# Kernel optimization log

Measured on AMD Instinct MI355X. Metric: run time of the kernel, lower is better.

## Reference

```python
import jax, jax.numpy as jnp
import numpy as np

B, T, N, D_IN, H, K, E, L = 32, 12, 2000, 2, 64, 2, 10, 2


def setup_inputs() -> dict:
    key = jax.random.key(0)
    ks = jax.random.split(key, 2 + 4 * L)
    s = 0.05
    inp = {
        "x": jax.random.normal(ks[0], (B, T, N, D_IN), jnp.float32),
        "node_embeddings": jax.random.normal(ks[1], (N, E), jnp.float32),
    }
    dims_in = [D_IN, H]
    for l in range(L):
        din = dims_in[l] + H  # cell input is concat([x_t, state])
        inp[f"gate_w{l}"] = jax.random.normal(ks[2 + 4 * l], (E, K, din, 2 * H), jnp.float32) * s
        inp[f"gate_b{l}"] = jax.random.normal(ks[3 + 4 * l], (E, 2 * H), jnp.float32) * s
        inp[f"upd_w{l}"] = jax.random.normal(ks[4 + 4 * l], (E, K, din, H), jnp.float32) * s
        inp[f"upd_b{l}"] = jax.random.normal(ks[5 + 4 * l], (E, H), jnp.float32) * s
    return inp


def _supports(node_embeddings):
    # adaptive adjacency from node embeddings + Chebyshev-style link polynomials
    A = jax.nn.softmax(jax.nn.relu(node_embeddings @ node_embeddings.T), axis=1)  # [N,N]
    sup = [jnp.eye(N, dtype=A.dtype), A]
    for _ in range(K - 2):
        sup.append(2.0 * (A @ sup[-1]) - sup[-2])
    return jnp.stack(sup)  # [K,N,N]


def _gconv(x, supports, emb, w_pool, b_pool):
    # x: [B,N,C] -> [B,N,O]; per-node weights generated from embeddings
    W = jnp.einsum('ne,ekio->nkio', emb, w_pool)          # [N,K,C,O]
    b = emb @ b_pool                                       # [N,O]
    xg = jnp.einsum('knm,bmc->bnkc', supports, x)          # graph aggregation
    return jnp.einsum('bnki,nkio->bno', xg, W) + b


def _cell(x_t, h, supports, emb, gw, gb, uw, ub):
    xs = jnp.concatenate([x_t, h], axis=-1)
    zr = jax.nn.sigmoid(_gconv(xs, supports, emb, gw, gb))
    z, r = jnp.split(zr, 2, axis=-1)
    hc = jnp.tanh(_gconv(jnp.concatenate([x_t, z * h], axis=-1), supports, emb, uw, ub))
    return r * h + (1.0 - r) * hc


def reference(x, node_embeddings, gate_w0, gate_b0, upd_w0, upd_b0,
              gate_w1, gate_b1, upd_w1, upd_b1):
    supports = _supports(node_embeddings)
    params = [(gate_w0, gate_b0, upd_w0, upd_b0),
              (gate_w1, gate_b1, upd_w1, upd_b1)]
    cur = x
    last = None
    for gw, gb, uw, ub in params:
        h0 = jnp.zeros((x.shape[0], N, H), x.dtype)

        def step(h, x_t, gw=gw, gb=gb, uw=uw, ub=ub):
            h_new = _cell(x_t, h, supports, node_embeddings, gw, gb, uw, ub)
            return h_new, h_new

        last, outs = jax.lax.scan(step, h0, jnp.swapaxes(cur, 0, 1))
        cur = jnp.swapaxes(outs, 0, 1)  # [B,T,N,H]
    # return_all_layers=False -> last layer's full sequence output and last state
    return cur, last
```

## Files before the change

kernel.cpp:

```cpp
#include <hip/hip_runtime.h>
#include <cstdint>

#define NN 2000
#define NP 2048
#define TT 12
#define BBATCH 32
#define HH 64
#define EE 10

typedef _Float16 f16;
typedef _Float16 f16x8 __attribute__((ext_vector_type(8)));
typedef float f32x4 __attribute__((ext_vector_type(4)));
typedef unsigned int u32;

__device__ __forceinline__ void gld_lds16(const void* g, void* lds) {
    __builtin_amdgcn_global_load_lds(
        (const __attribute__((address_space(1))) u32*)(const void*)g,
        (__attribute__((address_space(3))) u32*)(void*)lds, 16, 0, 0);
}

__global__ __launch_bounds__(256) void k_supports(const float* __restrict__ emb, f16* __restrict__ A2) {
    int n = blockIdx.x;
    int tid = threadIdx.x;
    if (n >= NN) {
        for (int m = tid; m < NP; m += 256) A2[(size_t)n * NP + m] = (f16)0.f;
        return;
    }
    __shared__ float red[4];
    float en[EE];
#pragma unroll
    for (int e = 0; e < EE; e++) en[e] = emb[n * EE + e];
    float g[8];
    float mx = 0.f;
#pragma unroll
    for (int i = 0; i < 8; i++) {
        int m = tid + 256 * i;
        float v = 0.f;
        if (m < NN) {
            float a = 0.f;
#pragma unroll
            for (int e = 0; e < EE; e++) a += en[e] * emb[m * EE + e];
            v = fmaxf(a, 0.f);
            mx = fmaxf(mx, v);
        }
        g[i] = v;
    }
#pragma unroll
    for (int d = 32; d; d >>= 1) mx = fmaxf(mx, __shfl_xor(mx, d));
    if ((tid & 63) == 0) red[tid >> 6] = mx;
    __syncthreads();
    mx = fmaxf(fmaxf(red[0], red[1]), fmaxf(red[2], red[3]));
    float s = 0.f;
#pragma unroll
    for (int i = 0; i < 8; i++) {
        int m = tid + 256 * i;
        if (m < NN) { g[i] = __expf(g[i] - mx); s += g[i]; }
    }
#pragma unroll
    for (int d = 32; d; d >>= 1) s += __shfl_xor(s, d);
    __syncthreads();
    if ((tid & 63) == 0) red[tid >> 6] = s;
    __syncthreads();
    s = red[0] + red[1] + red[2] + red[3];
    float inv = 1.f / s;
#pragma unroll
    for (int i = 0; i < 8; i++) {
        int m = tid + 256 * i;
        A2[(size_t)n * NP + m] = (m < NN) ? (f16)(g[i] * inv) : (f16)0.f;
    }
}

template <int DIN, int O>
__global__ __launch_bounds__(256) void k_wgen(const float* __restrict__ emb,
                                              const float* __restrict__ wpool,
                                              f16* __restrict__ WT) {
    constexpr int DPAD = (DIN == 66) ? 80 : 128;
    constexpr int R = 2 * DPAD;
    int n0 = blockIdx.x * 4;
    int r = threadIdx.x;
    if (r >= R) return;
    int k = (r >= DPAD) ? 1 : 0;
    int c = r - k * DPAD;
    bool valid = (c < DIN);
    float en[4][EE];
#pragma unroll
    for (int j = 0; j < 4; j++)
#pragma unroll
        for (int e = 0; e < EE; e++) en[j][e] = emb[(n0 + j) * EE + e];
    const float* wp = wpool + ((size_t)(k * DIN + (valid ? c : 0))) * O;
    for (int o = 0; o < O; o += 4) {
        float4 a[4] = {};
        if (valid) {
#pragma unroll
            for (int e = 0; e < EE; e++) {
                float4 w4 = *(const float4*)(wp + (size_t)e * 2 * DIN * O + o);
#pragma unroll
                for (int j = 0; j < 4; j++) {
                    a[j].x += en[j][e] * w4.x; a[j].y += en[j][e] * w4.y;
                    a[j].z += en[j][e] * w4.z; a[j].w += en[j][e] * w4.w;
                }
            }
        }
#pragma unroll
        for (int j = 0; j < 4; j++) {
            f16* outp = WT + ((size_t)(n0 + j) * O + o) * R + r;
            outp[0] = (f16)a[j].x; outp[(size_t)R] = (f16)a[j].y;
            outp[(size_t)2 * R] = (f16)a[j].z; outp[(size_t)3 * R] = (f16)a[j].w;
        }
    }
}

__global__ __launch_bounds__(256) void k_pack(const float* __restrict__ x, int t,
                                              f16* __restrict__ xs, f16* __restrict__ us) {
    int idx = blockIdx.x * 256 + threadIdx.x;
    if (idx >= BBATCH * 2 * NN) return;
    int n = idx % NN;
    int bd = idx / NN;
    int d = bd & 1, b = bd >> 1;
    float v = x[(((size_t)b * TT + t) * NN + n) * 2 + d];
    f16 h = (f16)v;
    xs[(size_t)n * (BBATCH * 66) + b * 66 + d] = h;
    us[(size_t)n * (BBATCH * 66) + b * 66 + d] = h;
}

template <int W>
__global__ __launch_bounds__(256) void k_tr(const f16* __restrict__ in, f16* __restrict__ out) {
    __shared__ f16 t[64][72];
    int bx = blockIdx.x, by = blockIdx.y;
    int tid = threadIdx.x;
    int ml = tid >> 2, q = tid & 3;
    int m = by * 64 + ml;
    f16x8 a, b2;
#pragma unroll
    for (int i = 0; i < 8; i++) { a[i] = (f16)0.f; b2[i] = (f16)0.f; }
    if (m < NN) {
        const f16* src = in + (size_t)m * W + bx * 64 + q * 16;
        a = *(const f16x8*)src;
        b2 = *(const f16x8*)(src + 8);
    }
    *(f16x8*)&t[ml][q * 16] = a;
    *(f16x8*)&t[ml][q * 16 + 8] = b2;
    __syncthreads();
    int jl = tid >> 2;
    f16x8 r0, r1;
#pragma unroll
    for (int i = 0; i < 8; i++) r0[i] = t[q * 16 + i][jl];
#pragma unroll
    for (int i = 0; i < 8; i++) r1[i] = t[q * 16 + 8 + i][jl];
    f16* dst = out + (size_t)(bx * 64 + jl) * NP + by * 64 + q * 16;
    *(f16x8*)dst = r0;
    *(f16x8*)(dst + 8) = r1;
}

template <int ST, int OFF>
__global__ __launch_bounds__(256) void k_gemm(const f16* __restrict__ A2, const f16* __restrict__ XT,
                                              f16* __restrict__ C, int J) {
    __shared__ __align__(16) f16 at[128 * 64];
    __shared__ __align__(16) f16 xt[64 * 64];
    int tj = blockIdx.x * 64;
    int tm = blockIdx.y * 128;
    int rowbase = (tj >> 6) * ST + OFF;
    int tid = threadIdx.x;
    int w = tid >> 6, l = tid & 63;
    int lr = l & 15, lg = l >> 4;
    f32x4 acc[2][4];
#pragma unroll
    for (int mt = 0; mt < 2; mt++)
#pragma unroll
        for (int nt = 0; nt < 4; nt++) acc[mt][nt] = (f32x4){0.f, 0.f, 0.f, 0.f};

    for (int k0 = 0; k0 < 2048; k0 += 64) {
#pragma unroll
        for (int i = 0; i < 4; i++) {
            int e = w * 2048 + i * 512 + l * 8;
            int row = e >> 6, s = (e >> 3) & 7;
            const f16* src = A2 + (size_t)(tm + row) * 2048 + k0 + ((s ^ (row & 7)) << 3);
            gld_lds16(src, &at[w * 2048 + i * 512]);
        }
#pragma unroll
        for (int i = 0; i < 2; i++) {
            int e = w * 1024 + i * 512 + l * 8;
            int row = e >> 6, s = (e >> 3) & 7;
            const f16* src = XT + (size_t)(rowbase + row) * 2048 + k0 + ((s ^ (row & 7)) << 3);
            gld_lds16(src, &xt[w * 1024 + i * 512]);
        }
        __syncthreads();
#pragma unroll
        for (int kk = 0; kk < 2; kk++) {
            int s = kk * 4 + lg;
            f16x8 av[2], bv[4];
#pragma unroll
            for (int mt = 0; mt < 2; mt++) {
                int row = w * 32 + mt * 16 + lr;
                av[mt] = *(const f16x8*)&at[row * 64 + ((s ^ (row & 7)) << 3)];
            }
#pragma unroll
            for (int nt = 0; nt < 4; nt++) {
                int row = nt * 16 + lr;
                bv[nt] = *(const f16x8*)&xt[row * 64 + ((s ^ (row & 7)) << 3)];
            }
#pragma unroll
            for (int mt = 0; mt < 2; mt++)
#pragma unroll
                for (int nt = 0; nt < 4; nt++)
                    acc[mt][nt] = __builtin_amdgcn_mfma_f32_16x16x32_f16(av[mt], bv[nt], acc[mt][nt], 0, 0, 0);
        }
        __syncthreads();
    }
#pragma unroll
    for (int mt = 0; mt < 2; mt++)
#pragma unroll
        for (int nt = 0; nt < 4; nt++)
#pragma unroll
            for (int q = 0; q < 4; q++) {
                int row = tm + w * 32 + mt * 16 + lg * 4 + q;
                int col = tj + nt * 16 + lr;
                C[(size_t)row * J + col] = (f16)acc[mt][nt][q];
            }
}

template <int L>
__global__ __launch_bounds__(256) void k_gate(const f16* __restrict__ xs_rm, const f16* __restrict__ agg,
                                              const f16* __restrict__ WT, const float* __restrict__ bpool,
                                              const float* __restrict__ emb, const float* __restrict__ hbuf,
                                              f16* __restrict__ us_rm, float* __restrict__ rbuf) {
    constexpr int DIN = L ? 128 : 66, CIN = L ? 64 : 2, DPAD = L ? 128 : 80;
    constexpr int R = 2 * DPAD, RPAD = R + 8, KCH = R / 32;
    constexpr int O = 128;
    int n = blockIdx.x;
    int tid = threadIdx.x, w = tid >> 6, l = tid & 63;
    int lr = l & 15, lg = l >> 4;
    __shared__ __align__(16) f16 xg[32 * RPAD];

    f16x8 wf[KCH][2];
    const f16* wbase = WT + (size_t)n * O * R;
#pragma unroll
    for (int kk = 0; kk < KCH; kk++)
#pragma unroll
        for (int nt = 0; nt < 2; nt++) {
            int o = w * 32 + nt * 16 + lr;
            wf[kk][nt] = *(const f16x8*)(wbase + (size_t)o * R + kk * 32 + lg * 8);
        }
    for (int i = tid; i < 32 * RPAD / 8; i += 256) *(float4*)&xg[i * 8] = (float4){0.f, 0.f, 0.f, 0.f};
    __syncthreads();
    if (L == 0) {
        for (int e = tid; e < 32 * DIN; e += 256) {
            int b = e / DIN, c = e % DIN;
            xg[b * RPAD + c] = xs_rm[(size_t)n * 32 * DIN + e];
            xg[b * RPAD + DPAD + c] = agg[(size_t)n * 32 * DIN + e];
        }
    } else {
        for (int e8 = tid; e8 < 32 * DIN / 8; e8 += 256) {
            int b = e8 >> 4, c8 = e8 & 15;
            *(f16x8*)&xg[b * RPAD + c8 * 8] = *(const f16x8*)&xs_rm[(size_t)n * 32 * DIN + e8 * 8];
            *(f16x8*)&xg[b * RPAD + DPAD + c8 * 8] = *(const f16x8*)&agg[(size_t)n * 32 * DIN + e8 * 8];
        }
    }
    __syncthreads();

    f32x4 acc[2][2];
#pragma unroll
    for (int mt = 0; mt < 2; mt++)
#pragma unroll
        for (int nt = 0; nt < 2; nt++) acc[mt][nt] = (f32x4){0.f, 0.f, 0.f, 0.f};
#pragma unroll
    for (int kk = 0; kk < KCH; kk++) {
        f16x8 av[2];
#pragma unroll
        for (int mt = 0; mt < 2; mt++)
            av[mt] = *(const f16x8*)&xg[(mt * 16 + lr) * RPAD + kk * 32 + lg * 8];
#pragma unroll
        for (int mt = 0; mt < 2; mt++)
#pragma unroll
            for (int nt = 0; nt < 2; nt++)
                acc[mt][nt] = __builtin_amdgcn_mfma_f32_16x16x32_f16(av[mt], wf[kk][nt], acc[mt][nt], 0, 0, 0);
    }
    float bias[2];
#pragma unroll
    for (int nt = 0; nt < 2; nt++) {
        int o = w * 32 + nt * 16 + lr;
        float bs = 0.f;
#pragma unroll
        for (int e = 0; e < EE; e++) bs += emb[n * EE + e] * bpool[e * 2 * HH + o];
        bias[nt] = bs;
    }
#pragma unroll
    for (int mt = 0; mt < 2; mt++)
#pragma unroll
        for (int nt = 0; nt < 2; nt++)
#pragma unroll
            for (int q = 0; q < 4; q++) {
                int o = w * 32 + nt * 16 + lr;
                int b = mt * 16 + lg * 4 + q;
                float v = acc[mt][nt][q] + bias[nt];
                float sg = 1.f / (1.f + __expf(-v));
                if (o < HH) {
                    float u = sg * hbuf[((size_t)n * 32 + b) * HH + o];
                    us_rm[(size_t)n * 32 * DIN + b * DIN + CIN + o] = (f16)u;
                } else {
                    rbuf[((size_t)n * 32 + b) * HH + (o - HH)] = sg;
                }
            }
}

template <int L>
__global__ __launch_bounds__(256) void k_upd(const f16* __restrict__ us_rm, const f16* __restrict__ agg,
                                             const f16* __restrict__ uagg, const f16* __restrict__ WT,
                                             const float* __restrict__ bpool, const float* __restrict__ emb,
                                             float* hbuf, const float* __restrict__ rbuf,
                                             f16* xs_self, f16* xsn, f16* usn,
                                             float* dout, int t) {
    constexpr int DIN = L ? 128 : 66, CIN = L ? 64 : 2, DPAD = L ? 128 : 80;
    constexpr int R = 2 * DPAD, RPAD = R + 8, KCH = R / 32;
    constexpr int O = 64;
    int n = blockIdx.x;
    int tid = threadIdx.x, w = tid >> 6, l = tid & 63;
    int lr = l & 15, lg = l >> 4;
    __shared__ __align__(16) f16 xg[32 * RPAD];

    f16x8 wf[KCH];
    const f16* wbase = WT + (size_t)n * O * R;
    int o = w * 16 + lr;
#pragma unroll
    for (int kk = 0; kk < KCH; kk++)
        wf[kk] = *(const f16x8*)(wbase + (size_t)o * R + kk * 32 + lg * 8);

    for (int i = tid; i < 32 * RPAD / 8; i += 256) *(float4*)&xg[i * 8] = (float4){0.f, 0.f, 0.f, 0.f};
    __syncthreads();
    if (L == 0) {
        for (int e = tid; e < 32 * DIN; e += 256) {
            int b = e / DIN, c = e % DIN;
            xg[b * RPAD + c] = us_rm[(size_t)n * 32 * DIN + e];
            f16 v = (c < CIN) ? agg[(size_t)n * 32 * DIN + b * DIN + c]
                              : uagg[(size_t)n * 32 * HH + b * HH + (c - CIN)];
            xg[b * RPAD + DPAD + c] = v;
        }
    } else {
        for (int e8 = tid; e8 < 32 * DIN / 8; e8 += 256) {
            int b = e8 >> 4, c8 = e8 & 15;
            *(f16x8*)&xg[b * RPAD + c8 * 8] = *(const f16x8*)&us_rm[(size_t)n * 32 * DIN + e8 * 8];
            f16x8 v = (c8 < 8) ? *(const f16x8*)&agg[(size_t)n * 32 * DIN + b * DIN + c8 * 8]
                               : *(const f16x8*)&uagg[(size_t)n * 32 * HH + b * HH + (c8 - 8) * 8];
            *(f16x8*)&xg[b * RPAD + DPAD + c8 * 8] = v;
        }
    }
    __syncthreads();

    f32x4 acc[2];
#pragma unroll
    for (int mt = 0; mt < 2; mt++) acc[mt] = (f32x4){0.f, 0.f, 0.f, 0.f};
#pragma unroll
    for (int kk = 0; kk < KCH; kk++) {
        f16x8 av[2];
#pragma unroll
        for (int mt = 0; mt < 2; mt++)
            av[mt] = *(const f16x8*)&xg[(mt * 16 + lr) * RPAD + kk * 32 + lg * 8];
#pragma unroll
        for (int mt = 0; mt < 2; mt++)
            acc[mt] = __builtin_amdgcn_mfma_f32_16x16x32_f16(av[mt], wf[kk], acc[mt], 0, 0, 0);
    }
    float bias = 0.f;
#pragma unroll
    for (int e = 0; e < EE; e++) bias += emb[n * EE + e] * bpool[e * HH + o];
#pragma unroll
    for (int mt = 0; mt < 2; mt++)
#pragma unroll
        for (int q = 0; q < 4; q++) {
            int b = mt * 16 + lg * 4 + q;
            float v = acc[mt][q] + bias;
            float ex = __expf(2.f * v);
            float hc = 1.f - 2.f / (ex + 1.f);
            size_t hidx = ((size_t)n * 32 + b) * HH + o;
            float r = rbuf[hidx], h = hbuf[hidx];
            float hn = r * h + (1.f - r) * hc;
            hbuf[hidx] = hn;
            f16 hh = (f16)hn;
            xs_self[(size_t)n * 32 * DIN + b * DIN + CIN + o] = hh;
            if (L == 0) {
                xsn[(size_t)n * 32 * 128 + b * 128 + o] = hh;
                usn[(size_t)n * 32 * 128 + b * 128 + o] = hh;
            } else {
                dout[(((size_t)b * TT + t) * NN + n) * HH + o] = hn;
                if (t == TT - 1)
                    dout[(size_t)BBATCH * TT * NN * HH + ((size_t)b * NN + n) * HH + o] = hn;
            }
        }
}

extern "C" void kernel_launch(void* const* d_in, const int* in_sizes, int n_in,
                              void* d_out, int out_size, void* d_ws, size_t ws_size,
                              hipStream_t stream) {
    (void)in_sizes; (void)n_in; (void)out_size; (void)ws_size;
    const float* x   = (const float*)d_in[0];
    const float* emb = (const float*)d_in[1];
    const float* gw0 = (const float*)d_in[2];
    const float* gb0 = (const float*)d_in[3];
    const float* uw0 = (const float*)d_in[4];
    const float* ub0 = (const float*)d_in[5];
    const float* gw1 = (const float*)d_in[6];
    const float* gb1 = (const float*)d_in[7];
    const float* uw1 = (const float*)d_in[8];
    const float* ub1 = (const float*)d_in[9];
    float* out = (float*)d_out;

    char* p = (char*)d_ws;
    auto alloc = [&](size_t bytes) { char* r = p; p += (bytes + 255) & ~(size_t)255; return r; };
    f16* A2    = (f16*)alloc((size_t)NP * NP * 2);
    f16* Wg0   = (f16*)alloc((size_t)NN * 128 * 160 * 2);
    f16* Wu0   = (f16*)alloc((size_t)NN * 64 * 160 * 2);
    f16* Wg1   = (f16*)alloc((size_t)NN * 128 * 256 * 2);
    f16* Wu1   = (f16*)alloc((size_t)NN * 64 * 256 * 2);
    f16* xs0   = (f16*)alloc((size_t)NN * 32 * 66 * 2);
    f16* xsT0  = (f16*)alloc((size_t)2112 * NP * 2);
    f16* agg0  = (f16*)alloc((size_t)NP * 2112 * 2);
    f16* us0   = (f16*)alloc((size_t)NN * 32 * 66 * 2);
    f16* usT0  = (f16*)alloc((size_t)2112 * NP * 2);
    f16* uagg0 = (f16*)alloc((size_t)NP * 2048 * 2);
    f16* xs1   = (f16*)alloc((size_t)NN * 32 * 128 * 2);
    f16* xsT1  = (f16*)alloc((size_t)4096 * NP * 2);
    f16* agg1  = (f16*)alloc((size_t)NP * 4096 * 2);
    f16* us1   = (f16*)alloc((size_t)NN * 32 * 128 * 2);
    f16* usT1  = (f16*)alloc((size_t)4096 * NP * 2);
    f16* uagg1 = (f16*)alloc((size_t)NP * 2048 * 2);
    float* h0  = (float*)alloc((size_t)NN * 32 * 64 * 4);
    float* r0  = (float*)alloc((size_t)NN * 32 * 64 * 4);
    float* h1  = (float*)alloc((size_t)NN * 32 * 64 * 4);
    float* r1  = (float*)alloc((size_t)NN * 32 * 64 * 4);

    hipMemsetAsync(xs0, 0, (size_t)NN * 32 * 66 * 2, stream);
    hipMemsetAsync(xs1, 0, (size_t)NN * 32 * 128 * 2, stream);
    hipMemsetAsync(h0, 0, (size_t)NN * 32 * 64 * 4, stream);
    hipMemsetAsync(h1, 0, (size_t)NN * 32 * 64 * 4, stream);

    k_supports<<<NP, 256, 0, stream>>>(emb, A2);
    k_wgen<66, 128><<<NN / 4, 256, 0, stream>>>(emb, gw0, Wg0);
    k_wgen<66, 64><<<NN / 4, 256, 0, stream>>>(emb, uw0, Wu0);
    k_wgen<128, 128><<<NN / 4, 256, 0, stream>>>(emb, gw1, Wg1);
    k_wgen<128, 64><<<NN / 4, 256, 0, stream>>>(emb, uw1, Wu1);

    for (int t = 0; t < TT; t++) {
        k_pack<<<500, 256, 0, stream>>>(x, t, xs0, us0);
        k_tr<2112><<<dim3(33, 32), 256, 0, stream>>>(xs0, xsT0);
        k_gemm<64, 0><<<dim3(2112 / 64, 16), 256, 0, stream>>>(A2, xsT0, agg0, 2112);
        k_gate<0><<<NN, 256, 0, stream>>>(xs0, agg0, Wg0, gb0, emb, h0, us0, r0);
        k_tr<2112><<<dim3(33, 32), 256, 0, stream>>>(us0, usT0);
        k_gemm<66, 2><<<dim3(2048 / 64, 16), 256, 0, stream>>>(A2, usT0, uagg0, 2048);
        k_upd<0><<<NN, 256, 0, stream>>>(us0, agg0, uagg0, Wu0, ub0, emb, h0, r0,
                                         xs0, xs1, us1, nullptr, t);
        k_tr<4096><<<dim3(64, 32), 256, 0, stream>>>(xs1, xsT1);
        k_gemm<64, 0><<<dim3(4096 / 64, 16), 256, 0, stream>>>(A2, xsT1, agg1, 4096);
        k_gate<1><<<NN, 256, 0, stream>>>(xs1, agg1, Wg1, gb1, emb, h1, us1, r1);
        k_tr<4096><<<dim3(64, 32), 256, 0, stream>>>(us1, usT1);
        k_gemm<128, 64><<<dim3(2048 / 64, 16), 256, 0, stream>>>(A2, usT1, uagg1, 2048);
        k_upd<1><<<NN, 256, 0, stream>>>(us1, agg1, uagg1, Wu1, ub1, emb, h1, r1,
                                         xs1, nullptr, nullptr, out, t);
    }
}
```

Baseline: 4.322 ms.

## Double-buffer LDS tiles in graph GEMM and swizzle blocks across XCDs

The GEMM kernel now uses two LDS buffers and prefetches the next K-slice via async global-to-LDS loads while MFMAs run on the current one. This removes one barrier per iteration. Block ids are also remapped so consecutive ids spread over the 8 XCDs, grouping tiles that share column panels for better L2 reuse. LDS use doubles, which may lower occupancy.

```diff
diff --git a/kernel.cpp b/kernel.cpp
--- a/kernel.cpp
+++ b/kernel.cpp
@@ -155,10 +155,13 @@
 template <int ST, int OFF>
 __global__ __launch_bounds__(256) void k_gemm(const f16* __restrict__ A2, const f16* __restrict__ XT,
                                               f16* __restrict__ C, int J) {
-    __shared__ __align__(16) f16 at[128 * 64];
-    __shared__ __align__(16) f16 xt[64 * 64];
-    int tj = blockIdx.x * 64;
-    int tm = blockIdx.y * 128;
+    __shared__ __align__(16) f16 at[2][128 * 64];
+    __shared__ __align__(16) f16 xt[2][64 * 64];
+    int id = blockIdx.x + gridDim.x * blockIdx.y;
+    int q = (gridDim.x * 16) >> 3;
+    int sid = (id & 7) * q + (id >> 3);
+    int tj = (sid >> 4) * 64;
+    int tm = (sid & 15) * 128;
     int rowbase = (tj >> 6) * ST + OFF;
     int tid = threadIdx.x;
     int w = tid >> 6, l = tid & 63;
@@ -169,22 +172,28 @@
 #pragma unroll
         for (int nt = 0; nt < 4; nt++) acc[mt][nt] = (f32x4){0.f, 0.f, 0.f, 0.f};
 
-    for (int k0 = 0; k0 < 2048; k0 += 64) {
+    auto stage = [&](int buf, int k0) {
 #pragma unroll
         for (int i = 0; i < 4; i++) {
             int e = w * 2048 + i * 512 + l * 8;
             int row = e >> 6, s = (e >> 3) & 7;
             const f16* src = A2 + (size_t)(tm + row) * 2048 + k0 + ((s ^ (row & 7)) << 3);
-            gld_lds16(src, &at[w * 2048 + i * 512]);
+            gld_lds16(src, &at[buf][w * 2048 + i * 512]);
         }
 #pragma unroll
         for (int i = 0; i < 2; i++) {
             int e = w * 1024 + i * 512 + l * 8;
             int row = e >> 6, s = (e >> 3) & 7;
             const f16* src = XT + (size_t)(rowbase + row) * 2048 + k0 + ((s ^ (row & 7)) << 3);
-            gld_lds16(src, &xt[w * 1024 + i * 512]);
-        }
-        __syncthreads();
+            gld_lds16(src, &xt[buf][w * 1024 + i * 512]);
+        }
+    };
+
+    stage(0, 0);
+    __syncthreads();
+    int cur = 0;
+    for (int k0 = 0; k0 < 2048; k0 += 64) {
+        if (k0 + 64 < 2048) stage(cur ^ 1, k0 + 64);
 #pragma unroll
         for (int kk = 0; kk < 2; kk++) {
             int s = kk * 4 + lg;
@@ -192,12 +201,12 @@
 #pragma unroll
             for (int mt = 0; mt < 2; mt++) {
                 int row = w * 32 + mt * 16 + lr;
-                av[mt] = *(const f16x8*)&at[row * 64 + ((s ^ (row & 7)) << 3)];
+                av[mt] = *(const f16x8*)&at[cur][row * 64 + ((s ^ (row & 7)) << 3)];
             }
 #pragma unroll
             for (int nt = 0; nt < 4; nt++) {
                 int row = nt * 16 + lr;
-                bv[nt] = *(const f16x8*)&xt[row * 64 + ((s ^ (row & 7)) << 3)];
+                bv[nt] = *(const f16x8*)&xt[cur][row * 64 + ((s ^ (row & 7)) << 3)];
             }
 #pragma unroll
             for (int mt = 0; mt < 2; mt++)
@@ -206,16 +215,17 @@
                     acc[mt][nt] = __builtin_amdgcn_mfma_f32_16x16x32_f16(av[mt], bv[nt], acc[mt][nt], 0, 0, 0);
         }
         __syncthreads();
+        cur ^= 1;
     }
 #pragma unroll
     for (int mt = 0; mt < 2; mt++)
 #pragma unroll
         for (int nt = 0; nt < 4; nt++)
 #pragma unroll
-            for (int q = 0; q < 4; q++) {
-                int row = tm + w * 32 + mt * 16 + lg * 4 + q;
+            for (int q2 = 0; q2 < 4; q2++) {
+                int row = tm + w * 32 + mt * 16 + lg * 4 + q2;
                 int col = tj + nt * 16 + lr;
-                C[(size_t)row * J + col] = (f16)acc[mt][nt][q];
+                C[(size_t)row * J + col] = (f16)acc[mt][nt][q2];
             }
 }
 
@@ -441,17 +451,17 @@
     for (int t = 0; t < TT; t++) {
         k_pack<<<500, 256, 0, stream>>>(x, t, xs0, us0);
         k_tr<2112><<<dim3(33, 32), 256, 0, stream>>>(xs0, xsT0);
-        k_gemm<64, 0><<<dim3(2112 / 64, 16), 256, 0, stream>>>(A2, xsT0, agg0, 2112);
+        k_gemm<64, 0><<<dim3(33, 16), 256, 0, stream>>>(A2, xsT0, agg0, 2112);
         k_gate<0><<<NN, 256, 0, stream>>>(xs0, agg0, Wg0, gb0, emb, h0, us0, r0);
         k_tr<2112><<<dim3(33, 32), 256, 0, stream>>>(us0, usT0);
-        k_gemm<66, 2><<<dim3(2048 / 64, 16), 256, 0, stream>>>(A2, usT0, uagg0, 2048);
+        k_gemm<66, 2><<<dim3(32, 16), 256, 0, stream>>>(A2, usT0, uagg0, 2048);
         k_upd<0><<<NN, 256, 0, stream>>>(us0, agg0, uagg0, Wu0, ub0, emb, h0, r0,
                                          xs0, xs1, us1, nullptr, t);
         k_tr<4096><<<dim3(64, 32), 256, 0, stream>>>(xs1, xsT1);
-        k_gemm<64, 0><<<dim3(4096 / 64, 16), 256, 0, stream>>>(A2, xsT1, agg1, 4096);
+        k_gemm<64, 0><<<dim3(64, 16), 256, 0, stream>>>(A2, xsT1, agg1, 4096);
         k_gate<1><<<NN, 256, 0, stream>>>(xs1, agg1, Wg1, gb1, emb, h1, us1, r1);
         k_tr<4096><<<dim3(64, 32), 256, 0, stream>>>(us1, usT1);
-        k_gemm<128, 64><<<dim3(2048 / 64, 16), 256, 0, stream>>>(A2, usT1, uagg1, 2048);
+        k_gemm<128, 64><<<dim3(32, 16), 256, 0, stream>>>(A2, usT1, uagg1, 2048);
         k_upd<1><<<NN, 256, 0, stream>>>(us1, agg1, uagg1, Wu1, ub1, emb, h1, r1,
                                          xs1, nullptr, nullptr, out, t);
     }
```

New measurement: 4.411 ms. 1.02x slower.

## Precompute input graph aggregation for all timesteps and reuse state aggregations

Applied to the files above, without the earlier changes.

Graph aggregation of the raw input x is hoisted out of the time loop into one GEMM over all 12 timesteps. The layer-0 state aggregation computed for layer 1's input is reused, and layer 1's hidden-state aggregation is computed at the end of each step for use in the next. This avoids aggregating the full concatenated input each step, so the per-step GEMMs shrink to 2048-wide state columns. In exchange it adds extra buffers and an extra transpose/GEMM pair per step, and the cross-step reuse of aggH1 relies on correct buffer ordering.

```diff
diff --git a/kernel.cpp b/kernel.cpp
--- a/kernel.cpp
+++ b/kernel.cpp
@@ -110,23 +110,19 @@
     }
 }
 
-__global__ __launch_bounds__(256) void k_pack(const float* __restrict__ x, int t,
-                                              f16* __restrict__ xs, f16* __restrict__ us) {
+__global__ __launch_bounds__(256) void k_xall(const float* __restrict__ x, f16* __restrict__ out) {
     int idx = blockIdx.x * 256 + threadIdx.x;
-    if (idx >= BBATCH * 2 * NN) return;
-    int n = idx % NN;
-    int bd = idx / NN;
-    int d = bd & 1, b = bd >> 1;
-    float v = x[(((size_t)b * TT + t) * NN + n) * 2 + d];
-    f16 h = (f16)v;
-    xs[(size_t)n * (BBATCH * 66) + b * 66 + d] = h;
-    us[(size_t)n * (BBATCH * 66) + b * 66 + d] = h;
-}
-
-template <int W>
+    if (idx >= 768 * NP) return;
+    int r = idx >> 11, n = idx & (NP - 1);
+    int t = r >> 6, rb = r & 63, b = rb >> 1, d = rb & 1;
+    float v = (n < NN) ? x[(((size_t)b * TT + t) * NN + n) * 2 + d] : 0.f;
+    out[idx] = (f16)v;
+}
+
+template <int W, int TS, int TO>
 __global__ __launch_bounds__(256) void k_tr(const f16* __restrict__ in, f16* __restrict__ out) {
     __shared__ f16 t[64][72];
-    int bx = blockIdx.x, by = blockIdx.y;
+    int ebx = blockIdx.x * TS + TO, by = blockIdx.y;
     int tid = threadIdx.x;
     int ml = tid >> 2, q = tid & 3;
     int m = by * 64 + ml;
@@ -134,7 +130,7 @@
 #pragma unroll
     for (int i = 0; i < 8; i++) { a[i] = (f16)0.f; b2[i] = (f16)0.f; }
     if (m < NN) {
-        const f16* src = in + (size_t)m * W + bx * 64 + q * 16;
+        const f16* src = in + (size_t)m * W + ebx * 64 + q * 16;
         a = *(const f16x8*)src;
         b2 = *(const f16x8*)(src + 8);
     }
@@ -147,7 +143,7 @@
     for (int i = 0; i < 8; i++) r0[i] = t[q * 16 + i][jl];
 #pragma unroll
     for (int i = 0; i < 8; i++) r1[i] = t[q * 16 + 8 + i][jl];
-    f16* dst = out + (size_t)(bx * 64 + jl) * NP + by * 64 + q * 16;
+    f16* dst = out + (size_t)(ebx * 64 + jl) * NP + by * 64 + q * 16;
     *(f16x8*)dst = r0;
     *(f16x8*)(dst + 8) = r1;
 }
@@ -219,14 +215,13 @@
             }
 }
 
-template <int L>
-__global__ __launch_bounds__(256) void k_gate(const f16* __restrict__ xs_rm, const f16* __restrict__ agg,
-                                              const f16* __restrict__ WT, const float* __restrict__ bpool,
-                                              const float* __restrict__ emb, const float* __restrict__ hbuf,
-                                              f16* __restrict__ us_rm, float* __restrict__ rbuf) {
-    constexpr int DIN = L ? 128 : 66, CIN = L ? 64 : 2, DPAD = L ? 128 : 80;
-    constexpr int R = 2 * DPAD, RPAD = R + 8, KCH = R / 32;
-    constexpr int O = 128;
+__global__ __launch_bounds__(256) void k_gate0(const float* __restrict__ x, int t,
+                                               const f16* __restrict__ h0rm, const f16* __restrict__ aggX,
+                                               const f16* __restrict__ aggH0, const f16* __restrict__ WT,
+                                               const float* __restrict__ bpool, const float* __restrict__ emb,
+                                               const float* __restrict__ hbuf,
+                                               f16* __restrict__ us_rm, float* __restrict__ rbuf) {
+    constexpr int DIN = 66, DPAD = 80, R = 160, RPAD = 168, KCH = 5, O = 128;
     int n = blockIdx.x;
     int tid = threadIdx.x, w = tid >> 6, l = tid & 63;
     int lr = l & 15, lg = l >> 4;
@@ -243,18 +238,14 @@
         }
     for (int i = tid; i < 32 * RPAD / 8; i += 256) *(float4*)&xg[i * 8] = (float4){0.f, 0.f, 0.f, 0.f};
     __syncthreads();
-    if (L == 0) {
-        for (int e = tid; e < 32 * DIN; e += 256) {
-            int b = e / DIN, c = e % DIN;
-            xg[b * RPAD + c] = xs_rm[(size_t)n * 32 * DIN + e];
-            xg[b * RPAD + DPAD + c] = agg[(size_t)n * 32 * DIN + e];
-        }
-    } else {
-        for (int e8 = tid; e8 < 32 * DIN / 8; e8 += 256) {
-            int b = e8 >> 4, c8 = e8 & 15;
-            *(f16x8*)&xg[b * RPAD + c8 * 8] = *(const f16x8*)&xs_rm[(size_t)n * 32 * DIN + e8 * 8];
-            *(f16x8*)&xg[b * RPAD + DPAD + c8 * 8] = *(const f16x8*)&agg[(size_t)n * 32 * DIN + e8 * 8];
-        }
+    for (int e = tid; e < 32 * DIN; e += 256) {
+        int b = e / DIN, c = e % DIN;
+        f16 v1 = (c < 2) ? (f16)x[(((size_t)b * TT + t) * NN + n) * 2 + c]
+                         : h0rm[(size_t)n * 2048 + b * 64 + (c - 2)];
+        f16 v2 = (c < 2) ? aggX[(size_t)n * 768 + t * 64 + b * 2 + c]
+                         : aggH0[(size_t)n * 2048 + b * 64 + (c - 2)];
+        xg[b * RPAD + c] = v1;
+        xg[b * RPAD + DPAD + c] = v2;
     }
     __syncthreads();
 
@@ -275,44 +266,37 @@
             for (int nt = 0; nt < 2; nt++)
                 acc[mt][nt] = __builtin_amdgcn_mfma_f32_16x16x32_f16(av[mt], wf[kk][nt], acc[mt][nt], 0, 0, 0);
     }
-    float bias[2];
-#pragma unroll
-    for (int nt = 0; nt < 2; nt++) {
-        int o = w * 32 + nt * 16 + lr;
-        float bs = 0.f;
-#pragma unroll
-        for (int e = 0; e < EE; e++) bs += emb[n * EE + e] * bpool[e * 2 * HH + o];
-        bias[nt] = bs;
-    }
-#pragma unroll
-    for (int mt = 0; mt < 2; mt++)
-#pragma unroll
-        for (int nt = 0; nt < 2; nt++)
+#pragma unroll
+    for (int mt = 0; mt < 2; mt++)
+#pragma unroll
+        for (int nt = 0; nt < 2; nt++) {
+            int o = w * 32 + nt * 16 + lr;
+            float bs = 0.f;
+#pragma unroll
+            for (int e = 0; e < EE; e++) bs += emb[n * EE + e] * bpool[e * 2 * HH + o];
 #pragma unroll
             for (int q = 0; q < 4; q++) {
-                int o = w * 32 + nt * 16 + lr;
                 int b = mt * 16 + lg * 4 + q;
-                float v = acc[mt][nt][q] + bias[nt];
+                float v = acc[mt][nt][q] + bs;
                 float sg = 1.f / (1.f + __expf(-v));
                 if (o < HH) {
                     float u = sg * hbuf[((size_t)n * 32 + b) * HH + o];
-                    us_rm[(size_t)n * 32 * DIN + b * DIN + CIN + o] = (f16)u;
+                    us_rm[(size_t)n * 2048 + b * 64 + o] = (f16)u;
                 } else {
                     rbuf[((size_t)n * 32 + b) * HH + (o - HH)] = sg;
                 }
             }
-}
-
-template <int L>
-__global__ __launch_bounds__(256) void k_upd(const f16* __restrict__ us_rm, const f16* __restrict__ agg,
-                                             const f16* __restrict__ uagg, const f16* __restrict__ WT,
-                                             const float* __restrict__ bpool, const float* __restrict__ emb,
-                                             float* hbuf, const float* __restrict__ rbuf,
-                                             f16* xs_self, f16* xsn, f16* usn,
-                                             float* dout, int t) {
-    constexpr int DIN = L ? 128 : 66, CIN = L ? 64 : 2, DPAD = L ? 128 : 80;
-    constexpr int R = 2 * DPAD, RPAD = R + 8, KCH = R / 32;
-    constexpr int O = 64;
+        }
+}
+
+__global__ __launch_bounds__(256) void k_upd0(const float* __restrict__ x, int t,
+                                              const f16* __restrict__ us0, const f16* __restrict__ aggX,
+                                              const f16* __restrict__ uagg, const f16* __restrict__ WT,
+                                              const float* __restrict__ bpool, const float* __restrict__ emb,
+                                              float* hbuf, const float* __restrict__ rbuf,
+                                              f16* __restrict__ h0rm, f16* __restrict__ xs1,
+                                              f16* __restrict__ us1) {
+    constexpr int DIN = 66, DPAD = 80, R = 160, RPAD = 168, KCH = 5, O = 64;
     int n = blockIdx.x;
     int tid = threadIdx.x, w = tid >> 6, l = tid & 63;
     int lr = l & 15, lg = l >> 4;
@@ -327,28 +311,20 @@
 
     for (int i = tid; i < 32 * RPAD / 8; i += 256) *(float4*)&xg[i * 8] = (float4){0.f, 0.f, 0.f, 0.f};
     __syncthreads();
-    if (L == 0) {
-        for (int e = tid; e < 32 * DIN; e += 256) {
-            int b = e / DIN, c = e % DIN;
-            xg[b * RPAD + c] = us_rm[(size_t)n * 32 * DIN + e];
-            f16 v = (c < CIN) ? agg[(size_t)n * 32 * DIN + b * DIN + c]
-                              : uagg[(size_t)n * 32 * HH + b * HH + (c - CIN)];
-            xg[b * RPAD + DPAD + c] = v;
-        }
-    } else {
-        for (int e8 = tid; e8 < 32 * DIN / 8; e8 += 256) {
-            int b = e8 >> 4, c8 = e8 & 15;
-            *(f16x8*)&xg[b * RPAD + c8 * 8] = *(const f16x8*)&us_rm[(size_t)n * 32 * DIN + e8 * 8];
-            f16x8 v = (c8 < 8) ? *(const f16x8*)&agg[(size_t)n * 32 * DIN + b * DIN + c8 * 8]
-                               : *(const f16x8*)&uagg[(size_t)n * 32 * HH + b * HH + (c8 - 8) * 8];
-            *(f16x8*)&xg[b * RPAD + DPAD + c8 * 8] = v;
-        }
+    for (int e = tid; e < 32 * DIN; e += 256) {
+        int b = e / DIN, c = e % DIN;
+        f16 v1 = (c < 2) ? (f16)x[(((size_t)b * TT + t) * NN + n) * 2 + c]
+                         : us0[(size_t)n * 2048 + b * 64 + (c - 2)];
+        f16 v2 = (c < 2) ? aggX[(size_t)n * 768 + t * 64 + b * 2 + c]
+                         : uagg[(size_t)n * 2048 + b * 64 + (c - 2)];
+        xg[b * RPAD + c] = v1;
+        xg[b * RPAD + DPAD + c] = v2;
     }
     __syncthreads();
 
     f32x4 acc[2];
-#pragma unroll
-    for (int mt = 0; mt < 2; mt++) acc[mt] = (f32x4){0.f, 0.f, 0.f, 0.f};
+    acc[0] = (f32x4){0.f, 0.f, 0.f, 0.f};
+    acc[1] = (f32x4){0.f, 0.f, 0.f, 0.f};
 #pragma unroll
     for (int kk = 0; kk < KCH; kk++) {
         f16x8 av[2];
@@ -375,15 +351,142 @@
             float hn = r * h + (1.f - r) * hc;
             hbuf[hidx] = hn;
             f16 hh = (f16)hn;
-            xs_self[(size_t)n * 32 * DIN + b * DIN + CIN + o] = hh;
-            if (L == 0) {
-                xsn[(size_t)n * 32 * 128 + b * 128 + o] = hh;
-                usn[(size_t)n * 32 * 128 + b * 128 + o] = hh;
-            } else {
-                dout[(((size_t)b * TT + t) * NN + n) * HH + o] = hn;
-                if (t == TT - 1)
-                    dout[(size_t)BBATCH * TT * NN * HH + ((size_t)b * NN + n) * HH + o] = hn;
+            h0rm[(size_t)n * 2048 + b * 64 + o] = hh;
+            xs1[(size_t)n * 4096 + b * 128 + o] = hh;
+            us1[(size_t)n * 4096 + b * 128 + o] = hh;
+        }
+}
+
+__global__ __launch_bounds__(256) void k_gate1(const f16* __restrict__ xs1,
+                                               const f16* __restrict__ aggA, const f16* __restrict__ aggB,
+                                               const f16* __restrict__ WT, const float* __restrict__ bpool,
+                                               const float* __restrict__ emb, const float* __restrict__ hbuf,
+                                               f16* __restrict__ us1, float* __restrict__ rbuf) {
+    constexpr int DPAD = 128, R = 256, RPAD = 264, KCH = 8, O = 128;
+    int n = blockIdx.x;
+    int tid = threadIdx.x, w = tid >> 6, l = tid & 63;
+    int lr = l & 15, lg = l >> 4;
+    __shared__ __align__(16) f16 xg[32 * RPAD];
+
+    f16x8 wf[KCH][2];
+    const f16* wbase = WT + (size_t)n * O * R;
+#pragma unroll
+    for (int kk = 0; kk < KCH; kk++)
+#pragma unroll
+        for (int nt = 0; nt < 2; nt++) {
+            int o = w * 32 + nt * 16 + lr;
+            wf[kk][nt] = *(const f16x8*)(wbase + (size_t)o * R + kk * 32 + lg * 8);
+        }
+    for (int e8 = tid; e8 < 32 * 16; e8 += 256) {
+        int b = e8 >> 4, c8 = e8 & 15;
+        *(f16x8*)&xg[b * RPAD + c8 * 8] = *(const f16x8*)&xs1[(size_t)n * 4096 + e8 * 8];
+        f16x8 v = (c8 < 8) ? *(const f16x8*)&aggA[(size_t)n * 2048 + b * 64 + c8 * 8]
+                           : *(const f16x8*)&aggB[(size_t)n * 2048 + b * 64 + (c8 - 8) * 8];
+        *(f16x8*)&xg[b * RPAD + DPAD + c8 * 8] = v;
+    }
+    __syncthreads();
+
+    f32x4 acc[2][2];
+#pragma unroll
+    for (int mt = 0; mt < 2; mt++)
+#pragma unroll
+        for (int nt = 0; nt < 2; nt++) acc[mt][nt] = (f32x4){0.f, 0.f, 0.f, 0.f};
+#pragma unroll
+    for (int kk = 0; kk < KCH; kk++) {
+        f16x8 av[2];
+#pragma unroll
+        for (int mt = 0; mt < 2; mt++)
+            av[mt] = *(const f16x8*)&xg[(mt * 16 + lr) * RPAD + kk * 32 + lg * 8];
+#pragma unroll
+        for (int mt = 0; mt < 2; mt++)
+#pragma unroll
+            for (int nt = 0; nt < 2; nt++)
+                acc[mt][nt] = __builtin_amdgcn_mfma_f32_16x16x32_f16(av[mt], wf[kk][nt], acc[mt][nt], 0, 0, 0);
+    }
+#pragma unroll
+    for (int mt = 0; mt < 2; mt++)
+#pragma unroll
+        for (int nt = 0; nt < 2; nt++) {
+            int o = w * 32 + nt * 16 + lr;
+            float bs = 0.f;
+#pragma unroll
+            for (int e = 0; e < EE; e++) bs += emb[n * EE + e] * bpool[e * 2 * HH + o];
+#pragma unroll
+            for (int q = 0; q < 4; q++) {
+                int b = mt * 16 + lg * 4 + q;
+                float v = acc[mt][nt][q] + bs;
+                float sg = 1.f / (1.f + __expf(-v));
+                if (o < HH) {
+                    float u = sg * hbuf[((size_t)n * 32 + b) * HH + o];
+                    us1[(size_t)n * 4096 + b * 128 + 64 + o] = (f16)u;
+                } else {
+                    rbuf[((size_t)n * 32 + b) * HH + (o - HH)] = sg;
+                }
             }
+        }
+}
+
+__global__ __launch_bounds__(256) void k_upd1(const f16* __restrict__ us1,
+                                              const f16* __restrict__ aggA, const f16* __restrict__ aggB,
+                                              const f16* __restrict__ WT, const float* __restrict__ bpool,
+                                              const float* __restrict__ emb,
+                                              float* hbuf, const float* __restrict__ rbuf,
+                                              f16* __restrict__ xs1, float* __restrict__ dout, int t) {
+    constexpr int DPAD = 128, R = 256, RPAD = 264, KCH = 8, O = 64;
+    int n = blockIdx.x;
+    int tid = threadIdx.x, w = tid >> 6, l = tid & 63;
+    int lr = l & 15, lg = l >> 4;
+    __shared__ __align__(16) f16 xg[32 * RPAD];
+
+    f16x8 wf[KCH];
+    const f16* wbase = WT + (size_t)n * O * R;
+    int o = w * 16 + lr;
+#pragma unroll
+    for (int kk = 0; kk < KCH; kk++)
+        wf[kk] = *(const f16x8*)(wbase + (size_t)o * R + kk * 32 + lg * 8);
+
+    for (int e8 = tid; e8 < 32 * 16; e8 += 256) {
+        int b = e8 >> 4, c8 = e8 & 15;
+        *(f16x8*)&xg[b * RPAD + c8 * 8] = *(const f16x8*)&us1[(size_t)n * 4096 + e8 * 8];
+        f16x8 v = (c8 < 8) ? *(const f16x8*)&aggA[(size_t)n * 2048 + b * 64 + c8 * 8]
+                           : *(const f16x8*)&aggB[(size_t)n * 2048 + b * 64 + (c8 - 8) * 8];
+        *(f16x8*)&xg[b * RPAD + DPAD + c8 * 8] = v;
+    }
+    __syncthreads();
+
+    f32x4 acc[2];
+    acc[0] = (f32x4){0.f, 0.f, 0.f, 0.f};
+    acc[1] = (f32x4){0.f, 0.f, 0.f, 0.f};
+#pragma unroll
+    for (int kk = 0; kk < KCH; kk++) {
+        f16x8 av[2];
+#pragma unroll
+        for (int mt = 0; mt < 2; mt++)
+            av[mt] = *(const f16x8*)&xg[(mt * 16 + lr) * RPAD + kk * 32 + lg * 8];
+#pragma unroll
+        for (int mt = 0; mt < 2; mt++)
+            acc[mt] = __builtin_amdgcn_mfma_f32_16x16x32_f16(av[mt], wf[kk], acc[mt], 0, 0, 0);
+    }
+    float bias = 0.f;
+#pragma unroll
+    for (int e = 0; e < EE; e++) bias += emb[n * EE + e] * bpool[e * HH + o];
+#pragma unroll
+    for (int mt = 0; mt < 2; mt++)
+#pragma unroll
+        for (int q = 0; q < 4; q++) {
+            int b = mt * 16 + lg * 4 + q;
+            float v = acc[mt][q] + bias;
+            float ex = __expf(2.f * v);
+            float hc = 1.f - 2.f / (ex + 1.f);
+            size_t hidx = ((size_t)n * 32 + b) * HH + o;
+            float r = rbuf[hidx], h = hbuf[hidx];
+            float hn = r * h + (1.f - r) * hc;
+            hbuf[hidx] = hn;
+            f16 hh = (f16)hn;
+            xs1[(size_t)n * 4096 + b * 128 + 64 + o] = hh;
+            dout[(((size_t)b * TT + t) * NN + n) * HH + o] = hn;
+            if (t == TT - 1)
+                dout[(size_t)BBATCH * TT * NN * HH + ((size_t)b * NN + n) * HH + o] = hn;
         }
 }
 
@@ -410,16 +513,17 @@
     f16* Wu0   = (f16*)alloc((size_t)NN * 64 * 160 * 2);
     f16* Wg1   = (f16*)alloc((size_t)NN * 128 * 256 * 2);
     f16* Wu1   = (f16*)alloc((size_t)NN * 64 * 256 * 2);
-    f16* xs0   = (f16*)alloc((size_t)NN * 32 * 66 * 2);
-    f16* xsT0  = (f16*)alloc((size_t)2112 * NP * 2);
-    f16* agg0  = (f16*)alloc((size_t)NP * 2112 * 2);
-    f16* us0   = (f16*)alloc((size_t)NN * 32 * 66 * 2);
-    f16* usT0  = (f16*)alloc((size_t)2112 * NP * 2);
+    f16* xTall = (f16*)alloc((size_t)768 * NP * 2);
+    f16* aggX  = (f16*)alloc((size_t)NP * 768 * 2);
+    f16* h0rm  = (f16*)alloc((size_t)NN * 2048 * 2);
+    f16* us0   = (f16*)alloc((size_t)NN * 2048 * 2);
+    f16* usT0  = (f16*)alloc((size_t)2048 * NP * 2);
     f16* uagg0 = (f16*)alloc((size_t)NP * 2048 * 2);
-    f16* xs1   = (f16*)alloc((size_t)NN * 32 * 128 * 2);
+    f16* aggH0 = (f16*)alloc((size_t)NP * 2048 * 2);
+    f16* aggH1 = (f16*)alloc((size_t)NP * 2048 * 2);
+    f16* xs1   = (f16*)alloc((size_t)NN * 4096 * 2);
     f16* xsT1  = (f16*)alloc((size_t)4096 * NP * 2);
-    f16* agg1  = (f16*)alloc((size_t)NP * 4096 * 2);
-    f16* us1   = (f16*)alloc((size_t)NN * 32 * 128 * 2);
+    f16* us1   = (f16*)alloc((size_t)NN * 4096 * 2);
     f16* usT1  = (f16*)alloc((size_t)4096 * NP * 2);
     f16* uagg1 = (f16*)alloc((size_t)NP * 2048 * 2);
     float* h0  = (float*)alloc((size_t)NN * 32 * 64 * 4);
@@ -427,8 +531,10 @@
     float* h1  = (float*)alloc((size_t)NN * 32 * 64 * 4);
     float* r1  = (float*)alloc((size_t)NN * 32 * 64 * 4);
 
-    hipMemsetAsync(xs0, 0, (size_t)NN * 32 * 66 * 2, stream);
-    hipMemsetAsync(xs1, 0, (size_t)NN * 32 * 128 * 2, stream);
+    hipMemsetAsync(h0rm, 0, (size_t)NN * 2048 * 2, stream);
+    hipMemsetAsync(xs1, 0, (size_t)NN * 4096 * 2, stream);
+    hipMemsetAsync(aggH0, 0, (size_t)NP * 2048 * 2, stream);
+    hipMemsetAsync(aggH1, 0, (size_t)NP * 2048 * 2, stream);
     hipMemsetAsync(h0, 0, (size_t)NN * 32 * 64 * 4, stream);
     hipMemsetAsync(h1, 0, (size_t)NN * 32 * 64 * 4, stream);
 
@@ -437,22 +543,23 @@
     k_wgen<66, 64><<<NN / 4, 256, 0, stream>>>(emb, uw0, Wu0);
     k_wgen<128, 128><<<NN / 4, 256, 0, stream>>>(emb, gw1, Wg1);
     k_wgen<128, 64><<<NN / 4, 256, 0, stream>>>(emb, uw1, Wu1);
+    k_xall<<<768 * NP / 256, 256, 0, stream>>>(x, xTall);
+    k_gemm<64, 0><<<dim3(12, 16), 256, 0, stream>>>(A2, xTall, aggX, 768);
 
     for (int t = 0; t < TT; t++) {
-        k_pack<<<500, 256, 0, stream>>>(x, t, xs0, us0);
-        k_tr<2112><<<dim3(33, 32), 256, 0, stream>>>(xs0, xsT0);
-        k_gemm<64, 0><<<dim3(2112 / 64, 16), 256, 0, stream>>>(A2, xsT0, agg0, 2112);
-        k_gate<0><<<NN, 256, 0, stream>>>(xs0, agg0, Wg0, gb0, emb, h0, us0, r0);
-        k_tr<2112><<<dim3(33, 32), 256, 0, stream>>>(us0, usT0);
-        k_gemm<66, 2><<<dim3(2048 / 64, 16), 256, 0, stream>>>(A2, usT0, uagg0, 2048);
-        k_upd<0><<<NN, 256, 0, stream>>>(us0, agg0, uagg0, Wu0, ub0, emb, h0, r0,
-                                         xs0, xs1, us1, nullptr, t);
-        k_tr<4096><<<dim3(64, 32), 256, 0, stream>>>(xs1, xsT1);
-        k_gemm<64, 0><<<dim3(4096 / 64, 16), 256, 0, stream>>>(A2, xsT1, agg1, 4096);
-        k_gate<1><<<NN, 256, 0, stream>>>(xs1, agg1, Wg1, gb1, emb, h1, us1, r1);
-        k_tr<4096><<<dim3(64, 32), 256, 0, stream>>>(us1, usT1);
-        k_gemm<128, 64><<<dim3(2048 / 64, 16), 256, 0, stream>>>(A2, usT1, uagg1, 2048);
-        k_upd<1><<<NN, 256, 0, stream>>>(us1, agg1, uagg1, Wu1, ub1, emb, h1, r1,
-                                         xs1, nullptr, nullptr, out, t);
-    }
-}
+        k_gate0<<<NN, 256, 0, stream>>>(x, t, h0rm, aggX, aggH0, Wg0, gb0, emb, h0, us0, r0);
+        k_tr<2048, 1, 0><<<dim3(32, 32), 256, 0, stream>>>(us0, usT0);
+        k_gemm<64, 0><<<dim3(32, 16), 256, 0, stream>>>(A2, usT0, uagg0, 2048);
+        k_upd0<<<NN, 256, 0, stream>>>(x, t, us0, aggX, uagg0, Wu0, ub0, emb, h0, r0,
+                                       h0rm, xs1, us1);
+        k_tr<4096, 2, 0><<<dim3(32, 32), 256, 0, stream>>>(xs1, xsT1);
+        k_gemm<128, 0><<<dim3(32, 16), 256, 0, stream>>>(A2, xsT1, aggH0, 2048);
+        k_gate1<<<NN, 256, 0, stream>>>(xs1, aggH0, aggH1, Wg1, gb1, emb, h1, us1, r1);
+        k_tr<4096, 2, 1><<<dim3(32, 32), 256, 0, stream>>>(us1, usT1);
+        k_gemm<128, 64><<<dim3(32, 16), 256, 0, stream>>>(A2, usT1, uagg1, 2048);
+        k_upd1<<<NN, 256, 0, stream>>>(us1, aggH0, uagg1, Wu1, ub1, emb, h1, r1,
+                                       xs1, out, t);
+        k_tr<4096, 2, 1><<<dim3(32, 32), 256, 0, stream>>>(xs1, xsT1);
+        k_gemm<128, 64><<<dim3(32, 16), 256, 0, stream>>>(A2, xsT1, aggH1, 2048);
+    }
+}
```

Result: faster. 4.036 ms (-6.6%).
